# Optimization experiments

Measured on AMD Instinct MI355X. Metric: run time of the kernel, lower is better.

## Reference

```python
import jax, jax.numpy as jnp
import numpy as np

B, N, M = 8, 2048, 16
HA, HB, HG = 64, 32, 32
NCONV, VOCAB, HINIT = 4, 100, 92
NAMINO = 2048
EPS = 1e-5


def setup_inputs() -> dict:
    key = jax.random.key(0)
    ks = jax.random.split(key, 24)
    s = 0.02
    return {
        'atom_emb_idx': jax.random.randint(ks[0], (B, N), 0, VOCAB, dtype=jnp.int32),
        'nbr_emb': jax.random.normal(ks[1], (B, N, M, HB), jnp.float32),
        'nbr_adj_list': jax.random.randint(ks[2], (B, N, M), 0, N, dtype=jnp.int32),
        'atom_amino_idx': jax.random.randint(ks[3], (B, N), 0, NAMINO, dtype=jnp.int32),
        'atom_mask': jnp.ones((B, N), jnp.float32),
        'embed_table': jax.random.normal(ks[4], (VOCAB, HINIT), jnp.float32) * s,
        'W_emb': jax.random.normal(ks[5], (HINIT, HA), jnp.float32) * s,
        'b_emb': jnp.zeros((HA,), jnp.float32),
        'fc_W': jax.random.normal(ks[6], (NCONV, 2 * HA + HB, 2 * HA), jnp.float32) * s,
        'fc_b': jnp.zeros((NCONV, 2 * HA), jnp.float32),
        'bnh_g': jnp.ones((NCONV, 2 * HA), jnp.float32),
        'bnh_b': jnp.zeros((NCONV, 2 * HA), jnp.float32),
        'bno_g': jnp.ones((NCONV, HA), jnp.float32),
        'bno_b': jnp.zeros((NCONV, HA), jnp.float32),
        'W_cf': jax.random.normal(ks[7], (HA, HG), jnp.float32) * s,
        'b_cf': jnp.zeros((HG,), jnp.float32),
        'W_out': jax.random.normal(ks[8], (HG, 1), jnp.float32) * s,
        'b_out': jnp.zeros((1,), jnp.float32),
        'W_af': jax.random.normal(ks[9], (HA, HG), jnp.float32) * s,
        'b_af': jnp.zeros((HG,), jnp.float32),
        'W_ao': jax.random.normal(ks[10], (HG, 1), jnp.float32) * s,
        'b_ao': jnp.zeros((1,), jnp.float32),
    }


def _bn(x, g, b, axes):
    # training-mode batchnorm (biased variance), matching torch default train()
    m = jnp.mean(x, axis=axes, keepdims=True)
    v = jnp.mean((x - m) ** 2, axis=axes, keepdims=True)
    return (x - m) * jax.lax.rsqrt(v + EPS) * g + b


def _conv(atom_emb, nbr_emb, adj, mask, W, b, g1, be1, g2, be2):
    # atom_emb [B,N,HA], adj [B,N,M], mask [B,N,1]
    nbr_atom = jax.vmap(lambda e, i: e[i])(atom_emb, adj)       # gather [B,N,M,HA]
    nbr_atom = nbr_atom * mask[..., None]                        # [B,N,1,1] bcast
    self_emb = jnp.broadcast_to(atom_emb[:, :, None, :], nbr_atom.shape)
    tot = jnp.concatenate([self_emb, nbr_atom, nbr_emb], axis=-1)  # [B,N,M,2HA+HB]
    z = tot @ W + b                                              # [B,N,M,2HA]
    z = _bn(z, g1, be1, (0, 1, 2))
    filt, core = jnp.split(z, 2, axis=-1)
    s = jnp.sum(jax.nn.sigmoid(filt) * jax.nn.relu(core), axis=2)  # [B,N,HA]
    s = _bn(s, g2, be2, (0, 1))
    return jax.nn.relu(atom_emb + s)


def reference(atom_emb_idx, nbr_emb, nbr_adj_list, atom_amino_idx, atom_mask,
              embed_table, W_emb, b_emb, fc_W, fc_b, bnh_g, bnh_b, bno_g, bno_b,
              W_cf, b_cf, W_out, b_out, W_af, b_af, W_ao, b_ao):
    atom_emb = embed_table[atom_emb_idx] @ W_emb + b_emb        # [B,N,HA]
    mask = atom_mask[..., None]                                  # [B,N,1]
    for i in range(NCONV):
        atom_emb = atom_emb * mask
        atom_emb = _conv(atom_emb, nbr_emb, nbr_adj_list, mask,
                         fc_W[i], fc_b[i], bnh_g[i], bnh_b[i], bno_g[i], bno_b[i])
    atom_emb = atom_emb * mask
    # residue (amino) pooling via scatter-add
    idx = atom_amino_idx.reshape(-1)
    amino_emb = jax.ops.segment_sum(atom_emb.reshape(-1, HA), idx, num_segments=NAMINO)
    mask_pooled = jnp.where(jnp.arange(NAMINO)[:, None] < jnp.min(idx), 0, 1).astype(jnp.uint8)
    amino_emb = jax.nn.relu(amino_emb) @ W_af + b_af
    amino_emb = jax.nn.relu(amino_emb)
    # protein pooling: masked mean
    protein_emb = jnp.sum(atom_emb, axis=1) / jnp.sum(mask, axis=1)  # [B,HA]
    protein_emb = jax.nn.relu(protein_emb) @ W_cf + b_cf
    protein_emb = jax.nn.relu(protein_emb)
    out_global = protein_emb @ W_out + b_out                     # [B,1]
    out_amino = amino_emb @ W_ao + b_ao                          # [NAMINO,1]
    return out_global, out_amino, mask_pooled
```

## Files before the change

### kernel.cpp

```cpp
#include <hip/hip_runtime.h>
#include <cstdint>
#include <cstddef>

#define EPS_ 1e-5f
#define NATOM 16384
#define NB    8
#define NN    2048
#define NM    16
#define NHA   64
#define NHB   32
#define NHG   32
#define NVOCAB 100
#define NHINIT 92
#define NAMINO_ 2048
#define NPART 1024
#define NSLOT 8

#define OFF_EMB      0
#define OFF_SELF     1048576
#define OFF_NBRU     3145728
#define OFF_S        4194304
#define OFF_AMINO    5242880
#define OFF_PSUM     5373952
#define OFF_MSUM     5374464
#define OFF_MAX      5374472
#define OFF_SLOT1    5374480
#define OFF_SLOT2    5382672
#define ZERO_FLOATS  (5386768 - 5242880)
#define OFF_PACK     5386768
#define OFF_WPACK    9581072
#define WS_FLOATS    9589264

typedef __attribute__((ext_vector_type(8))) short bf16x8;
typedef __attribute__((ext_vector_type(4))) float f32x4;

static __device__ __forceinline__ short f2bf(float f) {
    union { float f; uint32_t u; } v; v.f = f;
    uint32_t r = v.u + 0x7fffu + ((v.u >> 16) & 1u);
    return (short)(r >> 16);
}
static __device__ __forceinline__ float bfLo(uint32_t x) {
    union { uint32_t u; float f; } v; v.u = x << 16; return v.f;
}
static __device__ __forceinline__ float bfHi(uint32_t x) {
    union { uint32_t u; float f; } v; v.u = x & 0xffff0000u; return v.f;
}

static __device__ __forceinline__ int conv_wg(int bid) {
    return (bid & 7) * (NPART / 8) + (bid >> 3);
}

__launch_bounds__(256)
__global__ void k_prep(const float* __restrict__ nbr_emb, uint4* __restrict__ pack,
                       const int* __restrict__ atom_idx, const float* __restrict__ et,
                       const float* __restrict__ W_emb, const float* __restrict__ b_emb,
                       float* __restrict__ emb,
                       const float* __restrict__ fcW, uint4* __restrict__ wpack)
{
    __shared__ float lw[NHINIT * NHA];
    const int t = threadIdx.x;
    if (blockIdx.x < 4096) {
        int g = blockIdx.x * 256 + t;
        int bn = g >> 6, l = g & 63;
        const float* src = nbr_emb + (size_t)bn * 512 + (l & 15) * 32 + (l >> 4) * 8;
        float4 a = *reinterpret_cast<const float4*>(src);
        float4 b = *reinterpret_cast<const float4*>(src + 4);
        union { short s[8]; uint4 u; } o;
        o.s[0] = f2bf(a.x); o.s[1] = f2bf(a.y); o.s[2] = f2bf(a.z); o.s[3] = f2bf(a.w);
        o.s[4] = f2bf(b.x); o.s[5] = f2bf(b.y); o.s[6] = f2bf(b.z); o.s[7] = f2bf(b.w);
        pack[g] = o.u;
        return;
    }
    if (blockIdx.x >= 5120) {
        int L = blockIdx.x - 5120;
        if (t < 64) {
            int l15 = t & 15, lg = t >> 4;
            const float* We = fcW + (size_t)L * 160 * 128 + 128 * 128;
#pragma unroll
            for (int cb = 0; cb < 8; ++cb) {
                union { short s[8]; uint4 u; } w;
#pragma unroll
                for (int j = 0; j < 8; ++j)
                    w.s[j] = f2bf(We[(lg * 8 + j) * 128 + cb * 16 + l15]);
                wpack[L * 512 + cb * 64 + t] = w.u;
            }
        }
        return;
    }
    for (int j = t; j < NHINIT * NHA; j += 256) lw[j] = W_emb[j];
    __syncthreads();
    const int bbase = (blockIdx.x - 4096) * 16;
    const int sub = t >> 6, c = t & 63;
    const float bb = b_emb[c];
#pragma unroll
    for (int aa = 0; aa < 4; ++aa) {
        int atom = bbase + sub + 4 * aa;
        int idxu = __builtin_amdgcn_readfirstlane(atom_idx[atom]);
        const float* er = et + (size_t)idxu * NHINIT;
        float acc = bb;
        for (int h = 0; h < NHINIT; ++h)
            acc = fmaf(er[h], lw[h * NHA + c], acc);
        emb[(size_t)atom * NHA + c] = acc;
    }
}

template<int UPD>
__launch_bounds__(256)
__global__ void k_proj(float* __restrict__ emb, const float* __restrict__ mask,
                       const float* __restrict__ s_buf, const float* __restrict__ slot2,
                       const float* __restrict__ g1, const float* __restrict__ b1,
                       const float* __restrict__ fcW, const float* __restrict__ fcb,
                       float* __restrict__ selfp, uint32_t* __restrict__ nbrpU)
{
    __shared__ float le[512];
    __shared__ float nb[8][128];
    __shared__ float affA[64], affB[64];
    const int t = threadIdx.x;
    if (UPD) {
        if (t < 64) {
            float S = 0.f, Q = 0.f;
#pragma unroll
            for (int s = 0; s < NSLOT; ++s) {
                S += slot2[s * 128 + t];
                Q += slot2[s * 128 + 64 + t];
            }
            float mean = S * (1.f / 16384.f);
            float var = Q * (1.f / 16384.f) - mean * mean;
            float a = g1[t] * rsqrtf(var + EPS_);
            affA[t] = a; affB[t] = b1[t] - mean * a;
        }
        __syncthreads();
    }
#pragma unroll
    for (int jj = 0; jj < 2; ++jj) {
        int j = t + jj * 256;
        int gi = blockIdx.x * 512 + j;
        int bn = blockIdx.x * 8 + (j >> 6);
        int c = j & 63;
        float m = mask[bn];
        float v;
        if (UPD) {
            v = fmaxf(fmaf(s_buf[gi], affA[c], affB[c]) + emb[gi] * m, 0.f);
            emb[gi] = v;
        } else {
            v = emb[gi];
        }
        le[j] = v * m;
    }
    __syncthreads();
    int half = t >> 7;
    int tt = t & 127;
    int oc = half ? tt : (((tt & 7) << 4) | (tt >> 3));
    float acc[8];
    float bias = half ? 0.f : fcb[oc];
#pragma unroll
    for (int a = 0; a < 8; ++a) acc[a] = bias;
    const float* Wbase = fcW + (half * 64) * 128 + oc;
    for (int c = 0; c < 64; ++c) {
        float w = Wbase[c * 128];
#pragma unroll
        for (int a = 0; a < 8; ++a) acc[a] = fmaf(le[a * 64 + c], w, acc[a]);
    }
    if (half == 0) {
#pragma unroll
        for (int a = 0; a < 8; ++a)
            selfp[(size_t)(blockIdx.x * 8 + a) * 128 + tt] = acc[a];
    } else {
#pragma unroll
        for (int a = 0; a < 8; ++a) nb[a][oc] = acc[a];
    }
    __syncthreads();
#pragma unroll
    for (int k = 0; k < 2; ++k) {
        int idx = t + k * 256;
        int a = idx >> 6, s = idx & 63;
        int j = s >> 2, c2 = s & 3;
        int c = c2 * 16 + j;
        uint32_t lo = (uint16_t)f2bf(nb[a][c]);
        uint32_t hi = (uint16_t)f2bf(nb[a][c + 64]);
        nbrpU[(size_t)(blockIdx.x * 8 + a) * 64 + s] = lo | (hi << 16);
    }
}

__launch_bounds__(256, 4)
__global__ void k_conv_stats(const float* __restrict__ selfp, const uint32_t* __restrict__ nbrpU,
                             const uint4* __restrict__ pack, const int* __restrict__ adj,
                             const float* __restrict__ mask, const uint4* __restrict__ wpack,
                             float* __restrict__ slot1)
{
    __shared__ float red[4][256];
    const int lane = threadIdx.x & 63;
    const int wid = threadIdx.x >> 6;
    const int l15 = lane & 15, lg = lane >> 4;
    bf16x8 Wb[8];
#pragma unroll
    for (int cb = 0; cb < 8; ++cb) {
        union { uint4 u; bf16x8 v; } w;
        w.u = wpack[cb * 64 + lane];
        Wb[cb] = w.v;
    }
    float sum[8] = {0, 0, 0, 0, 0, 0, 0, 0};
    float sq[8] = {0, 0, 0, 0, 0, 0, 0, 0};
    const int wg = conv_wg(blockIdx.x);
    const int base = (wg * 4 + wid) * 4;
    const int adjv = adj[base * 16 + lane];
    for (int aa = 0; aa < 4; ++aa) {
        const int bn = base + aa;
        const int b = bn >> 11;
        const float mn = mask[bn];
        union { uint4 u; bf16x8 v; } af;
        af.u = pack[(size_t)bn * 64 + lane];
        const float4* spp = reinterpret_cast<const float4*>(selfp + (size_t)bn * 128 + l15 * 8);
        float4 sA = spp[0], sB = spp[1];
        float sp[8] = {sA.x, sA.y, sA.z, sA.w, sB.x, sB.y, sB.z, sB.w};
        const uint32_t* npb = nbrpU + (size_t)b * NN * 64;
        f32x4 acc[8];
#pragma unroll
        for (int r = 0; r < 4; ++r) {
            const int am = __shfl(adjv, aa * 16 + lg * 4 + r);
            const uint4 u4 = *reinterpret_cast<const uint4*>(npb + (size_t)am * 64 + l15 * 4);
            acc[0][r] = fmaf(mn, bfLo(u4.x), sp[0]); acc[4][r] = fmaf(mn, bfHi(u4.x), sp[4]);
            acc[1][r] = fmaf(mn, bfLo(u4.y), sp[1]); acc[5][r] = fmaf(mn, bfHi(u4.y), sp[5]);
            acc[2][r] = fmaf(mn, bfLo(u4.z), sp[2]); acc[6][r] = fmaf(mn, bfHi(u4.z), sp[6]);
            acc[3][r] = fmaf(mn, bfLo(u4.w), sp[3]); acc[7][r] = fmaf(mn, bfHi(u4.w), sp[7]);
        }
#pragma unroll
        for (int cb = 0; cb < 8; ++cb)
            acc[cb] = __builtin_amdgcn_mfma_f32_16x16x32_bf16(af.v, Wb[cb], acc[cb], 0, 0, 0);
#pragma unroll
        for (int cb = 0; cb < 8; ++cb) {
#pragma unroll
            for (int r = 0; r < 4; ++r) {
                float z = acc[cb][r];
                sum[cb] += z; sq[cb] = fmaf(z, z, sq[cb]);
            }
        }
    }
#pragma unroll
    for (int cb = 0; cb < 8; ++cb) {
        sum[cb] += __shfl_xor(sum[cb], 16);
        sum[cb] += __shfl_xor(sum[cb], 32);
        sq[cb] += __shfl_xor(sq[cb], 16);
        sq[cb] += __shfl_xor(sq[cb], 32);
    }
    if (lane < 16) {
#pragma unroll
        for (int cb = 0; cb < 8; ++cb) {
            red[wid][cb * 16 + lane] = sum[cb];
            red[wid][128 + cb * 16 + lane] = sq[cb];
        }
    }
    __syncthreads();
    const int t = threadIdx.x;
    float v = red[0][t] + red[1][t] + red[2][t] + red[3][t];
    atomicAdd(&slot1[(blockIdx.x & (NSLOT - 1)) * 256 + t], v);
}

__launch_bounds__(256, 4)
__global__ void k_conv_gate(const float* __restrict__ selfp, const uint32_t* __restrict__ nbrpU,
                            const uint4* __restrict__ pack, const int* __restrict__ adj,
                            const float* __restrict__ mask, const uint4* __restrict__ wpack,
                            const float* __restrict__ slot1,
                            const float* __restrict__ g0, const float* __restrict__ b0,
                            float* __restrict__ s_out, float* __restrict__ slot2)
{
    __shared__ float red[4][128];
    __shared__ float a1[128], b1s[128];
    const int t = threadIdx.x;
    if (t < 128) {
        float S = 0.f, Q = 0.f;
#pragma unroll
        for (int s = 0; s < NSLOT; ++s) {
            S += slot1[s * 256 + t];
            Q += slot1[s * 256 + 128 + t];
        }
        float mean = S * (1.f / 262144.f);
        float var = Q * (1.f / 262144.f) - mean * mean;
        float a = g0[t] * rsqrtf(var + EPS_);
        a1[t] = a; b1s[t] = b0[t] - mean * a;
    }
    __syncthreads();
    const int lane = threadIdx.x & 63;
    const int wid = threadIdx.x >> 6;
    const int l15 = lane & 15, lg = lane >> 4;
    bf16x8 Wb[8];
#pragma unroll
    for (int cb = 0; cb < 8; ++cb) {
        union { uint4 u; bf16x8 v; } w;
        w.u = wpack[cb * 64 + lane];
        Wb[cb] = w.v;
    }
    float aA[8], aB[8];
#pragma unroll
    for (int cb = 0; cb < 8; ++cb) {
        aA[cb] = a1[cb * 16 + l15];
        aB[cb] = b1s[cb * 16 + l15];
    }
    float ssum[4] = {0, 0, 0, 0}, ssq[4] = {0, 0, 0, 0};
    const int wg = conv_wg(blockIdx.x);
    const int base = (wg * 4 + wid) * 4;
    const int adjv = adj[base * 16 + lane];
    for (int aa = 0; aa < 4; ++aa) {
        const int bn = base + aa;
        const int b = bn >> 11;
        const float mn = mask[bn];
        union { uint4 u; bf16x8 v; } af;
        af.u = pack[(size_t)bn * 64 + lane];
        const float4* spp = reinterpret_cast<const float4*>(selfp + (size_t)bn * 128 + l15 * 8);
        float4 sA = spp[0], sB = spp[1];
        float sp[8] = {sA.x, sA.y, sA.z, sA.w, sB.x, sB.y, sB.z, sB.w};
        const uint32_t* npb = nbrpU + (size_t)b * NN * 64;
        f32x4 acc[8];
#pragma unroll
        for (int r = 0; r < 4; ++r) {
            const int am = __shfl(adjv, aa * 16 + lg * 4 + r);
            const uint4 u4 = *reinterpret_cast<const uint4*>(npb + (size_t)am * 64 + l15 * 4);
            acc[0][r] = fmaf(mn, bfLo(u4.x), sp[0]); acc[4][r] = fmaf(mn, bfHi(u4.x), sp[4]);
            acc[1][r] = fmaf(mn, bfLo(u4.y), sp[1]); acc[5][r] = fmaf(mn, bfHi(u4.y), sp[5]);
            acc[2][r] = fmaf(mn, bfLo(u4.z), sp[2]); acc[6][r] = fmaf(mn, bfHi(u4.z), sp[6]);
            acc[3][r] = fmaf(mn, bfLo(u4.w), sp[3]); acc[7][r] = fmaf(mn, bfHi(u4.w), sp[7]);
        }
#pragma unroll
        for (int cb = 0; cb < 8; ++cb)
            acc[cb] = __builtin_amdgcn_mfma_f32_16x16x32_bf16(af.v, Wb[cb], acc[cb], 0, 0, 0);
        float sv[4];
#pragma unroll
        for (int cb = 0; cb < 4; ++cb) {
            float s = 0.f;
#pragma unroll
            for (int r = 0; r < 4; ++r) {
                float zf = fmaf(acc[cb][r], aA[cb], aB[cb]);
                float zc = fmaf(acc[cb + 4][r], aA[cb + 4], aB[cb + 4]);
                float f = 1.f / (1.f + __expf(-zf));
                s = fmaf(f, fmaxf(zc, 0.f), s);
            }
            s += __shfl_xor(s, 16);
            s += __shfl_xor(s, 32);
            sv[cb] = s;
            ssum[cb] += s; ssq[cb] = fmaf(s, s, ssq[cb]);
        }
        if (lane < 16) {
#pragma unroll
            for (int cb = 0; cb < 4; ++cb)
                s_out[(size_t)bn * 64 + cb * 16 + lane] = sv[cb];
        }
    }
    if (lane < 16) {
#pragma unroll
        for (int cb = 0; cb < 4; ++cb) {
            red[wid][cb * 16 + lane] = ssum[cb];
            red[wid][64 + cb * 16 + lane] = ssq[cb];
        }
    }
    __syncthreads();
    if (t < 128) {
        float v = red[0][t] + red[1][t] + red[2][t] + red[3][t];
        atomicAdd(&slot2[(blockIdx.x & (NSLOT - 1)) * 128 + t], v);
    }
}

__launch_bounds__(256)
__global__ void k_pool(const float* __restrict__ emb, const float* __restrict__ s_buf,
                       const float* __restrict__ slot2,
                       const float* __restrict__ g1, const float* __restrict__ b1,
                       const float* __restrict__ mask, const int* __restrict__ aidx,
                       float* __restrict__ amino, float* __restrict__ psum,
                       float* __restrict__ msum, int* __restrict__ maxv)
{
    __shared__ float red[256];
    __shared__ float mred[4];
    __shared__ int kred[4];
    __shared__ float affA[64], affB[64];
    int t = threadIdx.x, sub = t >> 6, c = t & 63;
    if (t < 64) {
        float S = 0.f, Q = 0.f;
#pragma unroll
        for (int s = 0; s < NSLOT; ++s) {
            S += slot2[s * 128 + t];
            Q += slot2[s * 128 + 64 + t];
        }
        float mean = S * (1.f / 16384.f);
        float var = Q * (1.f / 16384.f) - mean * mean;
        float a = g1[t] * rsqrtf(var + EPS_);
        affA[t] = a; affB[t] = b1[t] - mean * a;
    }
    __syncthreads();
    int base = blockIdx.x * 32;
    int b = base >> 11;
    float pacc = 0.f, macc = 0.f;
    int kmax = 0;
    for (int j = 0; j < 8; ++j) {
        int bn = base + sub + 4 * j;
        size_t gi = (size_t)bn * 64 + c;
        float m = mask[bn];
        float e4 = fmaxf(fmaf(s_buf[gi], affA[c], affB[c]) + emb[gi] * m, 0.f);
        float v = e4 * m;
        int k = aidx[bn];
        atomicAdd(&amino[(size_t)k * 64 + c], v);
        pacc += v;
        if (c == 0) { macc += m; kmax = max(kmax, 0x7fffffff - k); }
    }
    red[t] = pacc;
    if (c == 0) { mred[sub] = macc; kred[sub] = kmax; }
    __syncthreads();
    if (t < 64) {
        float tot = red[t] + red[64 + t] + red[128 + t] + red[192 + t];
        atomicAdd(&psum[b * 64 + t], tot);
    }
    if (t == 0) {
        atomicAdd(&msum[b], mred[0] + mred[1] + mred[2] + mred[3]);
        atomicMax(maxv, max(max(kred[0], kred[1]), max(kred[2], kred[3])));
    }
}

__launch_bounds__(256)
__global__ void k_heads(const float* __restrict__ amino, const float* __restrict__ W_af,
                        const float* __restrict__ b_af, const float* __restrict__ W_ao,
                        const float* __restrict__ b_ao,
                        const float* __restrict__ psum, const float* __restrict__ msum,
                        const float* __restrict__ W_cf, const float* __restrict__ b_cf,
                        const float* __restrict__ W_out, const float* __restrict__ b_out,
                        const int* __restrict__ maxv, float* __restrict__ out)
{
    const int t = threadIdx.x;
    if (blockIdx.x < 256) {
        int kk = t >> 5, j = t & 31;
        int k = blockIdx.x * 8 + kk;
        float acc = b_af[j];
        for (int c = 0; c < 64; ++c)
            acc = fmaf(fmaxf(amino[(size_t)k * 64 + c], 0.f), W_af[c * 32 + j], acc);
        float h = fmaxf(acc, 0.f);
        float val = h * W_ao[j];
        for (int off = 16; off > 0; off >>= 1) val += __shfl_down(val, off, 32);
        if (j == 0) out[8 + k] = val + b_ao[0];
    } else if (blockIdx.x == 256) {
        int bb = t >> 5, j = t & 31;
        float inv = 1.f / msum[bb];
        float acc = b_cf[j];
        for (int c = 0; c < 64; ++c)
            acc = fmaf(fmaxf(psum[bb * 64 + c] * inv, 0.f), W_cf[c * 32 + j], acc);
        float h = fmaxf(acc, 0.f);
        float val = h * W_out[j];
        for (int off = 16; off > 0; off >>= 1) val += __shfl_down(val, off, 32);
        if (j == 0) out[bb] = val + b_out[0];
    } else {
        int k = (blockIdx.x - 257) * 256 + t;
        int minv = 0x7fffffff - *maxv;
        out[8 + NAMINO_ + k] = (k < minv) ? 0.f : 1.f;
    }
}

extern "C" void kernel_launch(void* const* d_in, const int* in_sizes, int n_in,
                              void* d_out, int out_size, void* d_ws, size_t ws_size,
                              hipStream_t stream)
{
    const int* atom_idx = (const int*)d_in[0];
    const float* nbr_emb = (const float*)d_in[1];
    const int* adj = (const int*)d_in[2];
    const int* aidx = (const int*)d_in[3];
    const float* mask = (const float*)d_in[4];
    const float* et = (const float*)d_in[5];
    const float* W_emb = (const float*)d_in[6];
    const float* b_emb = (const float*)d_in[7];
    const float* fcW = (const float*)d_in[8];
    const float* fcb = (const float*)d_in[9];
    const float* bnh_g = (const float*)d_in[10];
    const float* bnh_b = (const float*)d_in[11];
    const float* bno_g = (const float*)d_in[12];
    const float* bno_b = (const float*)d_in[13];
    const float* W_cf = (const float*)d_in[14];
    const float* b_cf = (const float*)d_in[15];
    const float* W_out = (const float*)d_in[16];
    const float* b_out = (const float*)d_in[17];
    const float* W_af = (const float*)d_in[18];
    const float* b_af = (const float*)d_in[19];
    const float* W_ao = (const float*)d_in[20];
    const float* b_ao = (const float*)d_in[21];

    float* ws = (float*)d_ws;
    float* emb = ws + OFF_EMB;
    float* selfp = ws + OFF_SELF;
    uint32_t* nbrpU = (uint32_t*)(ws + OFF_NBRU);
    float* s_buf = ws + OFF_S;
    float* amino = ws + OFF_AMINO;
    float* psum = ws + OFF_PSUM;
    float* msum = ws + OFF_MSUM;
    int* maxv = (int*)(ws + OFF_MAX);
    float* slot1 = ws + OFF_SLOT1;
    float* slot2 = ws + OFF_SLOT2;
    uint4* pack = (uint4*)(ws + OFF_PACK);
    uint4* wpack = (uint4*)(ws + OFF_WPACK);
    float* out = (float*)d_out;

    hipMemsetAsync(amino, 0, ZERO_FLOATS * sizeof(float), stream);

    k_prep<<<5124, 256, 0, stream>>>(nbr_emb, pack, atom_idx, et, W_emb, b_emb, emb,
                                     fcW, wpack);

    for (int i = 0; i < 4; ++i) {
        const float* Wi = fcW + (size_t)i * 160 * 128;
        if (i == 0)
            k_proj<0><<<NATOM / 8, 256, 0, stream>>>(emb, mask, s_buf, slot2, bno_g, bno_b,
                                                     Wi, fcb + i * 128, selfp, nbrpU);
        else
            k_proj<1><<<NATOM / 8, 256, 0, stream>>>(emb, mask, s_buf,
                                                     slot2 + (size_t)(i - 1) * (NSLOT * 128),
                                                     bno_g + (i - 1) * 64, bno_b + (i - 1) * 64,
                                                     Wi, fcb + i * 128, selfp, nbrpU);
        k_conv_stats<<<NPART, 256, 0, stream>>>(selfp, nbrpU, pack, adj, mask,
                                                wpack + (size_t)i * 512,
                                                slot1 + (size_t)i * (NSLOT * 256));
        k_conv_gate<<<NPART, 256, 0, stream>>>(selfp, nbrpU, pack, adj, mask,
                                               wpack + (size_t)i * 512,
                                               slot1 + (size_t)i * (NSLOT * 256),
                                               bnh_g + i * 128, bnh_b + i * 128,
                                               s_buf, slot2 + (size_t)i * (NSLOT * 128));
    }

    k_pool<<<NATOM / 32, 256, 0, stream>>>(emb, s_buf, slot2 + 3 * (NSLOT * 128),
                                           bno_g + 3 * 64, bno_b + 3 * 64,
                                           mask, aidx, amino, psum, msum, maxv);
    k_heads<<<265, 256, 0, stream>>>(amino, W_af, b_af, W_ao, b_ao,
                                     psum, msum, W_cf, b_cf, W_out, b_out, maxv, out);
}
```

Baseline: 273.1 us.

## Compute per-atom self/neighbor projections with bf16 MFMA using prepacked weights

Replaces the scalar FMA projection in k_proj with bf16 16x16x32 MFMA instructions, processing 16 atoms per block instead of 8. The fc weights for the self and neighbor halves are pre-packed into bf16 MFMA fragment layout once in k_prep, using extra blocks. This aims to cut the ALU and LDS cost of the projection kernel that runs four times. In exchange, the inputs and self projections are rounded to bf16 before accumulation, which lowers precision, and the selfp stores become more scattered.

New measurement: 238.5 us. -12.7%, faster.

```diff
diff --git a/kernel.cpp b/kernel.cpp
--- a/kernel.cpp
+++ b/kernel.cpp
@@ -29,7 +29,8 @@
 #define ZERO_FLOATS  (5386768 - 5242880)
 #define OFF_PACK     5386768
 #define OFF_WPACK    9581072
-#define WS_FLOATS    9589264
+#define OFF_WPACK2   9589264
+#define WS_FLOATS    9622032
 
 typedef __attribute__((ext_vector_type(8))) short bf16x8;
 typedef __attribute__((ext_vector_type(4))) float f32x4;
@@ -55,7 +56,8 @@
                        const int* __restrict__ atom_idx, const float* __restrict__ et,
                        const float* __restrict__ W_emb, const float* __restrict__ b_emb,
                        float* __restrict__ emb,
-                       const float* __restrict__ fcW, uint4* __restrict__ wpack)
+                       const float* __restrict__ fcW, uint4* __restrict__ wpack,
+                       uint4* __restrict__ wpack2)
 {
     __shared__ float lw[NHINIT * NHA];
     const int t = threadIdx.x;
@@ -71,6 +73,22 @@
         pack[g] = o.u;
         return;
     }
+    if (blockIdx.x >= 5124) {
+        int L = blockIdx.x - 5124;
+        if (t < 64) {
+            const float* WL = fcW + (size_t)L * 160 * 128;
+            for (int f = 0; f < 32; ++f) {
+                int h = f >> 4, ks = (f >> 3) & 1, cb = f & 7;
+                union { short s[8]; uint4 u; } w;
+#pragma unroll
+                for (int j = 0; j < 8; ++j)
+                    w.s[j] = f2bf(WL[(h * 64 + ks * 32 + (t >> 4) * 8 + j) * 128
+                                     + cb * 16 + (t & 15)]);
+                wpack2[L * 2048 + f * 64 + t] = w.u;
+            }
+        }
+        return;
+    }
     if (blockIdx.x >= 5120) {
         int L = blockIdx.x - 5120;
         if (t < 64) {
@@ -109,11 +127,10 @@
 __global__ void k_proj(float* __restrict__ emb, const float* __restrict__ mask,
                        const float* __restrict__ s_buf, const float* __restrict__ slot2,
                        const float* __restrict__ g1, const float* __restrict__ b1,
-                       const float* __restrict__ fcW, const float* __restrict__ fcb,
+                       const uint4* __restrict__ wp, const float* __restrict__ fcb,
                        float* __restrict__ selfp, uint32_t* __restrict__ nbrpU)
 {
-    __shared__ float le[512];
-    __shared__ float nb[8][128];
+    __shared__ __align__(16) unsigned short lexb[16][72];
     __shared__ float affA[64], affB[64];
     const int t = threadIdx.x;
     if (UPD) {
@@ -132,12 +149,12 @@
         __syncthreads();
     }
 #pragma unroll
-    for (int jj = 0; jj < 2; ++jj) {
-        int j = t + jj * 256;
-        int gi = blockIdx.x * 512 + j;
-        int bn = blockIdx.x * 8 + (j >> 6);
-        int c = j & 63;
-        float m = mask[bn];
+    for (int k = 0; k < 4; ++k) {
+        int idx = t + k * 256;
+        int a = idx >> 6, c = idx & 63;
+        int gi = blockIdx.x * 1024 + idx;
+        int atom = blockIdx.x * 16 + a;
+        float m = mask[atom];
         float v;
         if (UPD) {
             v = fmaxf(fmaf(s_buf[gi], affA[c], affB[c]) + emb[gi] * m, 0.f);
@@ -145,40 +162,45 @@
         } else {
             v = emb[gi];
         }
-        le[j] = v * m;
-    }
-    __syncthreads();
-    int half = t >> 7;
-    int tt = t & 127;
-    int oc = half ? tt : (((tt & 7) << 4) | (tt >> 3));
-    float acc[8];
-    float bias = half ? 0.f : fcb[oc];
-#pragma unroll
-    for (int a = 0; a < 8; ++a) acc[a] = bias;
-    const float* Wbase = fcW + (half * 64) * 128 + oc;
-    for (int c = 0; c < 64; ++c) {
-        float w = Wbase[c * 128];
-#pragma unroll
-        for (int a = 0; a < 8; ++a) acc[a] = fmaf(le[a * 64 + c], w, acc[a]);
-    }
-    if (half == 0) {
-#pragma unroll
-        for (int a = 0; a < 8; ++a)
-            selfp[(size_t)(blockIdx.x * 8 + a) * 128 + tt] = acc[a];
-    } else {
-#pragma unroll
-        for (int a = 0; a < 8; ++a) nb[a][oc] = acc[a];
-    }
-    __syncthreads();
-#pragma unroll
-    for (int k = 0; k < 2; ++k) {
-        int idx = t + k * 256;
-        int a = idx >> 6, s = idx & 63;
-        int j = s >> 2, c2 = s & 3;
-        int c = c2 * 16 + j;
-        uint32_t lo = (uint16_t)f2bf(nb[a][c]);
-        uint32_t hi = (uint16_t)f2bf(nb[a][c + 64]);
-        nbrpU[(size_t)(blockIdx.x * 8 + a) * 64 + s] = lo | (hi << 16);
+        lexb[a][c] = (unsigned short)f2bf(v * m);
+    }
+    __syncthreads();
+    const int lane = t & 63, w = t >> 6;
+    const int l15 = lane & 15, lg = lane >> 4;
+    const unsigned short* ap = &lexb[l15][lg * 8];
+    union { uint4 u; bf16x8 v; } a0, a1;
+    a0.u = *reinterpret_cast<const uint4*>(ap);
+    a1.u = *reinterpret_cast<const uint4*>(ap + 32);
+    union { uint4 u; bf16x8 v; } B[2][2][2];
+#pragma unroll
+    for (int h = 0; h < 2; ++h)
+#pragma unroll
+        for (int cbi = 0; cbi < 2; ++cbi)
+#pragma unroll
+            for (int ks = 0; ks < 2; ++ks)
+                B[h][cbi][ks].u = wp[(h * 16 + ks * 8 + (w + cbi * 4)) * 64 + lane];
+    float bias0 = fcb[w * 16 + l15];
+    float bias4 = fcb[(w + 4) * 16 + l15];
+    f32x4 aS0 = {bias0, bias0, bias0, bias0};
+    f32x4 aS4 = {bias4, bias4, bias4, bias4};
+    f32x4 aN0 = {0.f, 0.f, 0.f, 0.f};
+    f32x4 aN4 = {0.f, 0.f, 0.f, 0.f};
+    aS0 = __builtin_amdgcn_mfma_f32_16x16x32_bf16(a0.v, B[0][0][0].v, aS0, 0, 0, 0);
+    aS0 = __builtin_amdgcn_mfma_f32_16x16x32_bf16(a1.v, B[0][0][1].v, aS0, 0, 0, 0);
+    aS4 = __builtin_amdgcn_mfma_f32_16x16x32_bf16(a0.v, B[0][1][0].v, aS4, 0, 0, 0);
+    aS4 = __builtin_amdgcn_mfma_f32_16x16x32_bf16(a1.v, B[0][1][1].v, aS4, 0, 0, 0);
+    aN0 = __builtin_amdgcn_mfma_f32_16x16x32_bf16(a0.v, B[1][0][0].v, aN0, 0, 0, 0);
+    aN0 = __builtin_amdgcn_mfma_f32_16x16x32_bf16(a1.v, B[1][0][1].v, aN0, 0, 0, 0);
+    aN4 = __builtin_amdgcn_mfma_f32_16x16x32_bf16(a0.v, B[1][1][0].v, aN4, 0, 0, 0);
+    aN4 = __builtin_amdgcn_mfma_f32_16x16x32_bf16(a1.v, B[1][1][1].v, aN4, 0, 0, 0);
+#pragma unroll
+    for (int r = 0; r < 4; ++r) {
+        size_t atomg = (size_t)blockIdx.x * 16 + lg * 4 + r;
+        selfp[atomg * 128 + l15 * 8 + w] = aS0[r];
+        selfp[atomg * 128 + l15 * 8 + w + 4] = aS4[r];
+        uint32_t lo = (uint16_t)f2bf(aN0[r]);
+        uint32_t hi = (uint16_t)f2bf(aN4[r]);
+        nbrpU[atomg * 64 + l15 * 4 + w] = lo | (hi << 16);
     }
 }
 
@@ -490,23 +512,24 @@
     float* slot2 = ws + OFF_SLOT2;
     uint4* pack = (uint4*)(ws + OFF_PACK);
     uint4* wpack = (uint4*)(ws + OFF_WPACK);
+    uint4* wpack2 = (uint4*)(ws + OFF_WPACK2);
     float* out = (float*)d_out;
 
     hipMemsetAsync(amino, 0, ZERO_FLOATS * sizeof(float), stream);
 
-    k_prep<<<5124, 256, 0, stream>>>(nbr_emb, pack, atom_idx, et, W_emb, b_emb, emb,
-                                     fcW, wpack);
+    k_prep<<<5128, 256, 0, stream>>>(nbr_emb, pack, atom_idx, et, W_emb, b_emb, emb,
+                                     fcW, wpack, wpack2);
 
     for (int i = 0; i < 4; ++i) {
-        const float* Wi = fcW + (size_t)i * 160 * 128;
+        const uint4* wp2 = wpack2 + (size_t)i * 2048;
         if (i == 0)
-            k_proj<0><<<NATOM / 8, 256, 0, stream>>>(emb, mask, s_buf, slot2, bno_g, bno_b,
-                                                     Wi, fcb + i * 128, selfp, nbrpU);
+            k_proj<0><<<NATOM / 16, 256, 0, stream>>>(emb, mask, s_buf, slot2, bno_g, bno_b,
+                                                      wp2, fcb + i * 128, selfp, nbrpU);
         else
-            k_proj<1><<<NATOM / 8, 256, 0, stream>>>(emb, mask, s_buf,
-                                                     slot2 + (size_t)(i - 1) * (NSLOT * 128),
-                                                     bno_g + (i - 1) * 64, bno_b + (i - 1) * 64,
-                                                     Wi, fcb + i * 128, selfp, nbrpU);
+            k_proj<1><<<NATOM / 16, 256, 0, stream>>>(emb, mask, s_buf,
+                                                      slot2 + (size_t)(i - 1) * (NSLOT * 128),
+                                                      bno_g + (i - 1) * 64, bno_b + (i - 1) * 64,
+                                                      wp2, fcb + i * 128, selfp, nbrpU);
         k_conv_stats<<<NPART, 256, 0, stream>>>(selfp, nbrpU, pack, adj, mask,
                                                 wpack + (size_t)i * 512,
                                                 slot1 + (size_t)i * (NSLOT * 256));
```
